# Performance work log

Hardware: AMD Instinct MI355X
Metric: run time of the kernel (lower is better)

The kernel has to match this reference:

```python
import jax, jax.numpy as jnp
import numpy as np

B, S, E, H = 64, 50, 512, 1024
VS, VT, T = 32000, 32000, 50
PAD = 0


def setup_inputs() -> dict:
    key = jax.random.key(0)
    ks = jax.random.split(key, 20)
    p = lambda k, shape: (jax.random.normal(k, shape, dtype=jnp.float32) * 0.02)
    inp = {
        "source_batch": jax.random.randint(ks[0], (B, S), 0, VS),
        "source_lengths": jax.random.randint(ks[1], (B,), 0, S),
        "batch_positions": jax.random.randint(ks[2], (B, S), 0, S + 1),
        "target_batch": jax.random.randint(ks[3], (B, T), 0, VT),
        # encoder params
        "enc_emb": p(ks[4], (VS, E)),
        "pos_emb": p(ks[5], (S + 1, E)),
        "cat_W": p(ks[6], (E, 2 * E)),
        "cat_b": p(ks[7], (E,)),
        "scale_W": p(ks[8], (H, E)),
        "scale_b": p(ks[9], (H,)),
        # decoder params
        "dec_emb": p(ks[10], (VT, E)),
        "attn_W": p(ks[11], (1, H + E)),
        "attn_b": p(ks[12], (1,)),
        "W_ih": p(ks[13], (4 * H, 2 * E)),
        "W_hh": p(ks[14], (4 * H, H)),
        "b_ih": p(ks[15], (4 * H,)),
        "b_hh": p(ks[16], (4 * H,)),
        "proj_W": p(ks[17], (VT, H)),
        "proj_b": p(ks[18], (VT,)),
    }
    return inp


def _forward(source_batch, batch_positions, target_batch,
             enc_emb, pos_emb, cat_W, cat_b, scale_W, scale_b,
             dec_emb, attn_W, attn_b, W_ih, W_hh, b_ih, b_hh, proj_W, proj_b):
    # ---- Encoder (GRU is unused in the original forward; dropout = eval identity)
    words = enc_emb[source_batch]            # (B,S,E)
    pos = pos_emb[batch_positions]           # (B,S,E)
    cat = jnp.concatenate([words, pos], axis=2)            # (B,S,2E)
    enc_out = cat @ cat_W.T + cat_b                         # (B,S,E)
    avg = jnp.mean(enc_out, axis=1)                         # (B,E)
    h0 = jax.nn.relu(avg @ scale_W.T + scale_b)             # (B,H)
    pad_mask = (source_batch == PAD)[..., None]             # (B,S,1)

    Hd = h0.shape[1]

    def step(carry, tok):
        h, c = carry                                        # (B,H), (B,H)
        w = dec_emb[tok]                                    # (B,E)
        rep_h = jnp.broadcast_to(h[:, None, :], (h.shape[0], S, Hd))
        attn_in = jnp.concatenate([enc_out, rep_h], axis=2)  # (B,S,E+H)
        scores = attn_in @ attn_W.T + attn_b                 # (B,S,1)
        aw = jax.nn.softmax(scores, axis=1)                  # softmax over S
        aw = jnp.where(pad_mask, 0.0, aw)
        aw = aw / jnp.sum(aw, axis=1, keepdims=True)
        ctx = jnp.sum(aw * enc_out, axis=1)                  # (B,E)
        x = jnp.concatenate([w, ctx], axis=1)                # (B,2E)
        gates = x @ W_ih.T + b_ih + h @ W_hh.T + b_hh        # (B,4H)
        i, f, g, o = jnp.split(gates, 4, axis=1)
        i, f, o = jax.nn.sigmoid(i), jax.nn.sigmoid(f), jax.nn.sigmoid(o)
        g = jnp.tanh(g)
        c_new = f * c + i * g
        h_new = o * jnp.tanh(c_new)
        logits = h_new @ proj_W.T + proj_b                   # (B,VT)
        return (h_new, c_new), logits

    toks = target_batch[:, : T - 1].T                        # (T-1, B)
    _, logits = jax.lax.scan(step, (h0, h0), toks)
    return logits                                            # (T-1, B, VT)


def reference(source_batch, source_lengths, batch_positions, target_batch,
              enc_emb, pos_emb, cat_W, cat_b, scale_W, scale_b,
              dec_emb, attn_W, attn_b, W_ih, W_hh, b_ih, b_hh, proj_W, proj_b):
    del source_lengths  # only used for max_len, which is unused downstream
    return _forward(source_batch, batch_positions, target_batch,
                    enc_emb, pos_emb, cat_W, cat_b, scale_W, scale_b,
                    dec_emb, attn_W, attn_b, W_ih, W_hh, b_ih, b_hh, proj_W, proj_b)
```

## Files before the change

kernel.cpp:

```cpp
#include <hip/hip_runtime.h>
#include <hip/hip_bf16.h>


typedef __attribute__((ext_vector_type(8))) short bf16x8;
typedef __attribute__((ext_vector_type(4))) short short4v;
typedef __attribute__((ext_vector_type(4))) float f32x4;

__device__ __forceinline__ short f2b(float f) {
    union { float f; unsigned u; } x;
    x.f = f;
    unsigned r = (x.u + 0x7FFFu + ((x.u >> 16) & 1u)) >> 16;
    return (short)r;
}
__device__ __forceinline__ float b2f(short s) {
    union { unsigned u; float f; } x;
    x.u = ((unsigned)(unsigned short)s) << 16;
    return x.f;
}

__global__ __launch_bounds__(256)
void cvt_kernel(const float* __restrict__ in, short* __restrict__ out, int n4) {
    int i = blockIdx.x * 256 + threadIdx.x;
    if (i < n4) {
        float4 x = ((const float4*)in)[i];
        short4v v;
        v[0] = f2b(x.x); v[1] = f2b(x.y); v[2] = f2b(x.z); v[3] = f2b(x.w);
        ((short4v*)out)[i] = v;
    }
}

template <int MODE>
__global__ __launch_bounds__(256, 2)
void gemm_bt(const float* __restrict__ Af, const float* __restrict__ Af2,
             const short* __restrict__ Ab,
             const int* __restrict__ idx1, const int* __restrict__ idx2,
             const short* __restrict__ Bt,
             const float* __restrict__ bias1, const float* __restrict__ bias2,
             float* __restrict__ Out) {
    constexpr int OUTS = (MODE == 0) ? 512 : ((MODE == 1) ? 4096 : 32000);

    __shared__ short As[128 * 32];
    __shared__ short Bs[128 * 32];

    const int tid = threadIdx.x;
    const int lane = tid & 63;
    const int wave = tid >> 6;
    const int wm = wave >> 1, wn = wave & 1;
    const int quad = lane >> 4;
    const int l15 = lane & 15;
    const int tm = blockIdx.y * 128;
    const int tn = blockIdx.x * 128;

    f32x4 acc[4][4];
    const f32x4 vzero = {0.f, 0.f, 0.f, 0.f};
#pragma unroll
    for (int mi = 0; mi < 4; mi++)
#pragma unroll
        for (int ni = 0; ni < 4; ni++) acc[mi][ni] = vzero;

    const int c0 = tid, c1 = tid + 256;
    const int r0 = c0 >> 2, r1 = c1 >> 2;
    const int o0 = (c0 & 3) * 8, o1 = (c1 & 3) * 8;

    const float *a0_lo = nullptr, *a0_hi = nullptr, *a1_lo = nullptr, *a1_hi = nullptr;
    const short *ab0 = nullptr, *ab1 = nullptr;
    if constexpr (MODE == 0) {
        const int g0 = tm + r0, g1 = tm + r1;
        a0_lo = Af + idx1[g0] * 512;
        a0_hi = Af2 + idx2[g0] * 512 - 512;
        a1_lo = Af + idx1[g1] * 512;
        a1_hi = Af2 + idx2[g1] * 512 - 512;
    } else if constexpr (MODE == 1) {
        int g0 = tm + r0; if (g0 > 3135) g0 = 3135;
        int g1 = tm + r1; if (g1 > 3135) g1 = 3135;
        a0_lo = Af + idx1[(g0 & 63) * 50 + (g0 >> 6)] * 512;
        a0_hi = Af2 + (g0 & 63) * 512 - 512;
        a1_lo = Af + idx1[(g1 & 63) * 50 + (g1 >> 6)] * 512;
        a1_hi = Af2 + (g1 & 63) * 512 - 512;
    } else {
        ab0 = Ab + (tm + r0) * 1024;
        ab1 = Ab + (tm + r1) * 1024;
    }
    const short* pb0 = Bt + (tn + r0) * 1024;
    const short* pb1 = Bt + (tn + r1) * 1024;

    for (int k0 = 0; k0 < 1024; k0 += 32) {
        const int ka0 = k0 + o0, ka1 = k0 + o1;
        bf16x8 va0, va1;
        if constexpr (MODE == 2) {
            va0 = *(const bf16x8*)(ab0 + ka0);
            va1 = *(const bf16x8*)(ab1 + ka1);
        } else {
            const float* p0 = (ka0 < 512) ? (a0_lo + ka0) : (a0_hi + ka0);
            const float* p1 = (ka1 < 512) ? (a1_lo + ka1) : (a1_hi + ka1);
            float4 x0 = *(const float4*)p0, y0 = *(const float4*)(p0 + 4);
            float4 x1 = *(const float4*)p1, y1 = *(const float4*)(p1 + 4);
            va0[0] = f2b(x0.x); va0[1] = f2b(x0.y); va0[2] = f2b(x0.z); va0[3] = f2b(x0.w);
            va0[4] = f2b(y0.x); va0[5] = f2b(y0.y); va0[6] = f2b(y0.z); va0[7] = f2b(y0.w);
            va1[0] = f2b(x1.x); va1[1] = f2b(x1.y); va1[2] = f2b(x1.z); va1[3] = f2b(x1.w);
            va1[4] = f2b(y1.x); va1[5] = f2b(y1.y); va1[6] = f2b(y1.z); va1[7] = f2b(y1.w);
        }
        bf16x8 vb0 = *(const bf16x8*)(pb0 + ka0);
        bf16x8 vb1 = *(const bf16x8*)(pb1 + ka1);

        __syncthreads();
        *(bf16x8*)&As[r0 * 32 + o0] = va0;
        *(bf16x8*)&As[r1 * 32 + o1] = va1;
        *(bf16x8*)&Bs[r0 * 32 + o0] = vb0;
        *(bf16x8*)&Bs[r1 * 32 + o1] = vb1;
        __syncthreads();

        bf16x8 af[4], bfr[4];
#pragma unroll
        for (int mi = 0; mi < 4; mi++)
            af[mi] = *(const bf16x8*)&As[(wm * 64 + mi * 16 + l15) * 32 + quad * 8];
#pragma unroll
        for (int ni = 0; ni < 4; ni++)
            bfr[ni] = *(const bf16x8*)&Bs[(wn * 64 + ni * 16 + l15) * 32 + quad * 8];
#pragma unroll
        for (int mi = 0; mi < 4; mi++)
#pragma unroll
            for (int ni = 0; ni < 4; ni++)
                acc[mi][ni] = __builtin_amdgcn_mfma_f32_16x16x32_bf16(
                    af[mi], bfr[ni], acc[mi][ni], 0, 0, 0);
    }

    const int gm_base = tm + wm * 64;
    const int gn_base = tn + wn * 64;
#pragma unroll
    for (int mi = 0; mi < 4; mi++) {
#pragma unroll
        for (int ni = 0; ni < 4; ni++) {
            const int gn = gn_base + ni * 16 + l15;
            float bias = bias1[gn];
            if constexpr (MODE == 1) bias += bias2[gn];
#pragma unroll
            for (int r = 0; r < 4; r++) {
                const int gm = gm_base + mi * 16 + quad * 4 + r;
                float v = acc[mi][ni][r] + bias;
                if constexpr (MODE == 0) {
                    Out[gm * OUTS + gn] = v;
                } else {
                    if (gm < 3136) Out[gm * OUTS + gn] = v;
                }
            }
        }
    }
}

__global__ __launch_bounds__(256)
void h0_kernel(const float* __restrict__ enc, const float* __restrict__ sW,
               const float* __restrict__ sb, short* __restrict__ h0out,
               float* __restrict__ cst) {
    __shared__ float avg[512];
    const int b = blockIdx.x;
    const int tid = threadIdx.x;
    for (int e = tid; e < 512; e += 256) {
        float s = 0.f;
        for (int ss = 0; ss < 50; ss++) s += enc[(b * 50 + ss) * 512 + e];
        avg[e] = s * (1.0f / 50.0f);
    }
    __syncthreads();
    for (int r = tid; r < 1024; r += 256) {
        float s = sb[r];
        const float* wr = sW + r * 512;
        for (int e = 0; e < 512; e++) s += avg[e] * wr[e];
        s = fmaxf(s, 0.f);
        h0out[b * 1024 + r] = f2b(s);
        cst[b * 1024 + r] = s;
    }
}

__global__ __launch_bounds__(256)
void attn_kernel(const float* __restrict__ enc, const float* __restrict__ attn_W,
                 const int* __restrict__ src, float* __restrict__ ctx) {
    __shared__ float wE[512];
    __shared__ float part[64][4];
    __shared__ float aws[64];
    const int b = blockIdx.x;
    const int tid = threadIdx.x;
    for (int e = tid; e < 512; e += 256) wE[e] = attn_W[e];
    __syncthreads();
    const int ss = tid >> 2, q = tid & 3;
    float p = 0.f;
    if (ss < 50) {
        const float* row = enc + (b * 50 + ss) * 512;
        for (int e = q * 128; e < q * 128 + 128; e++) p += row[e] * wE[e];
    }
    part[ss][q] = p;
    __syncthreads();
    if (tid < 64) aws[tid] = part[tid][0] + part[tid][1] + part[tid][2] + part[tid][3];
    __syncthreads();
    if (tid == 0) {
        float mx = -1e30f;
        for (int s = 0; s < 50; s++) mx = fmaxf(mx, aws[s]);
        float sum = 0.f;
        for (int s = 0; s < 50; s++) {
            float v = (src[b * 50 + s] == 0) ? 0.f : expf(aws[s] - mx);
            aws[s] = v;
            sum += v;
        }
        float inv = 1.f / sum;
        for (int s = 0; s < 50; s++) aws[s] *= inv;
    }
    __syncthreads();
    for (int e = tid; e < 512; e += 256) {
        float s = 0.f;
        for (int ss2 = 0; ss2 < 50; ss2++) s += aws[ss2] * enc[(b * 50 + ss2) * 512 + e];
        ctx[b * 512 + e] = s;
    }
}

__global__ __launch_bounds__(256)
void lstm_step(const short* __restrict__ hprev, short* __restrict__ hnext,
               const float* __restrict__ pre_t, const short* __restrict__ whh,
               float* __restrict__ cst) {
    __shared__ float gsm[16 * 64];
    const int tid = threadIdx.x;
    const int lane = tid & 63;
    const int w = tid >> 6;
    const int quad = lane >> 4;
    const int l15 = lane & 15;
    const int j0 = blockIdx.x * 4;

    const short* arow = whh + ((l15 >> 2) * 1024 + j0 + (l15 & 3)) * 1024;
    const short* brow = hprev + (w * 16 + l15) * 1024;
    f32x4 acc = {0.f, 0.f, 0.f, 0.f};
#pragma unroll
    for (int k0 = 0; k0 < 1024; k0 += 32) {
        bf16x8 a = *(const bf16x8*)(arow + k0 + quad * 8);
        bf16x8 bb = *(const bf16x8*)(brow + k0 + quad * 8);
        acc = __builtin_amdgcn_mfma_f32_16x16x32_bf16(a, bb, acc, 0, 0, 0);
    }
#pragma unroll
    for (int r = 0; r < 4; r++) gsm[(quad * 4 + r) * 64 + w * 16 + l15] = acc[r];
    __syncthreads();

    const int b = tid & 63;
    const int jl = tid >> 6;
    const int j = j0 + jl;
    float gi = gsm[(0 + jl) * 64 + b] + pre_t[b * 4096 + j];
    float gf = gsm[(4 + jl) * 64 + b] + pre_t[b * 4096 + 1024 + j];
    float gg = gsm[(8 + jl) * 64 + b] + pre_t[b * 4096 + 2048 + j];
    float go = gsm[(12 + jl) * 64 + b] + pre_t[b * 4096 + 3072 + j];
    float iv = 1.f / (1.f + expf(-gi));
    float fv = 1.f / (1.f + expf(-gf));
    float gv = tanhf(gg);
    float ov = 1.f / (1.f + expf(-go));
    const int ci = b * 1024 + j;
    float cn = fv * cst[ci] + iv * gv;
    cst[ci] = cn;
    hnext[ci] = f2b(ov * tanhf(cn));
}

extern "C" void kernel_launch(void* const* d_in, const int* in_sizes, int n_in,
                              void* d_out, int out_size, void* d_ws, size_t ws_size,
                              hipStream_t stream) {
    (void)in_sizes; (void)n_in; (void)out_size; (void)ws_size;

    const int* src = (const int*)d_in[0];
    const int* pos = (const int*)d_in[2];
    const int* tgt = (const int*)d_in[3];
    const float* enc_emb = (const float*)d_in[4];
    const float* pos_emb = (const float*)d_in[5];
    const float* cat_W = (const float*)d_in[6];
    const float* cat_b = (const float*)d_in[7];
    const float* scale_W = (const float*)d_in[8];
    const float* scale_b = (const float*)d_in[9];
    const float* dec_emb = (const float*)d_in[10];
    const float* attn_W = (const float*)d_in[11];
    const float* W_ih = (const float*)d_in[13];
    const float* W_hh = (const float*)d_in[14];
    const float* b_ih = (const float*)d_in[15];
    const float* b_hh = (const float*)d_in[16];
    const float* proj_W = (const float*)d_in[17];
    const float* proj_b = (const float*)d_in[18];
    float* out = (float*)d_out;

    char* ws = (char*)d_ws;
    short* H_ALL = (short*)(ws + 0);
    float* ENCO  = (float*)(ws + 6684672);
    float* CST   = (float*)(ws + 13238272);
    float* CTX   = (float*)(ws + 13500416);
    float* PRE   = (float*)(ws + 13631488);
    short* CATW  = (short*)(ws + 65011712);
    short* WIH   = (short*)(ws + 66060288);
    short* WHH   = (short*)(ws + 74448896);
    short* PROJ  = (short*)(ws + 82837504);

    cvt_kernel<<<512, 256, 0, stream>>>(cat_W, CATW, 131072);
    cvt_kernel<<<4096, 256, 0, stream>>>(W_ih, WIH, 1048576);
    cvt_kernel<<<4096, 256, 0, stream>>>(W_hh, WHH, 1048576);
    cvt_kernel<<<32000, 256, 0, stream>>>(proj_W, PROJ, 8192000);

    gemm_bt<0><<<dim3(4, 25), 256, 0, stream>>>(enc_emb, pos_emb, nullptr, src, pos,
                                                CATW, cat_b, nullptr, ENCO);
    h0_kernel<<<64, 256, 0, stream>>>(ENCO, scale_W, scale_b, H_ALL, CST);
    attn_kernel<<<64, 256, 0, stream>>>(ENCO, attn_W, src, CTX);
    gemm_bt<1><<<dim3(32, 25), 256, 0, stream>>>(dec_emb, CTX, nullptr, tgt, nullptr,
                                                 WIH, b_ih, b_hh, PRE);
    for (int t = 0; t < 49; t++)
        lstm_step<<<256, 256, 0, stream>>>(H_ALL + t * 65536, H_ALL + (t + 1) * 65536,
                                           PRE + t * 64 * 4096, WHH, CST);
    gemm_bt<2><<<dim3(250, 25), 256, 0, stream>>>(nullptr, nullptr, H_ALL + 65536,
                                                  nullptr, nullptr, PROJ, proj_b, nullptr, out);
}
```

Before: 1.631 ms.

## Use direct global-to-LDS loads, XCD-aware tile swizzle, and vectorize h0 dot product

Loads of the bf16 B tiles, and of the A tiles in mode 2, now go straight from global memory into LDS through global_load_lds. This skips the round trip through registers. Block-to-tile mapping for the gate and projection GEMMs is remapped so consecutive blocks on the same XCD share tiles, aiming at better L2 reuse. The h0 kernel's dot product is vectorized with float4 loads. The direct LDS loads are issued after the barrier, so their latency is no longer overlapped with the previous iteration, and the swizzle arithmetic assumes fixed grid sizes.

```diff
diff --git a/kernel.cpp b/kernel.cpp
--- a/kernel.cpp
+++ b/kernel.cpp
@@ -12,10 +12,12 @@
     unsigned r = (x.u + 0x7FFFu + ((x.u >> 16) & 1u)) >> 16;
     return (short)r;
 }
-__device__ __forceinline__ float b2f(short s) {
-    union { unsigned u; float f; } x;
-    x.u = ((unsigned)(unsigned short)s) << 16;
-    return x.f;
+
+__device__ __forceinline__ void gload16(const short* g, short* l) {
+    __builtin_amdgcn_global_load_lds(
+        (const __attribute__((address_space(1))) unsigned int*)g,
+        (__attribute__((address_space(3))) unsigned int*)l,
+        16, 0, 0);
 }
 
 __global__ __launch_bounds__(256)
@@ -48,8 +50,22 @@
     const int wm = wave >> 1, wn = wave & 1;
     const int quad = lane >> 4;
     const int l15 = lane & 15;
-    const int tm = blockIdx.y * 128;
-    const int tn = blockIdx.x * 128;
+
+    int mt, nt;
+    if constexpr (MODE == 0) {
+        mt = blockIdx.y; nt = blockIdx.x;
+    } else if constexpr (MODE == 1) {
+        const int f = blockIdx.y * 32 + blockIdx.x;
+        const int g = (f & 7) * 100 + (f >> 3);
+        mt = g % 25; nt = g / 25;
+    } else {
+        const int f = blockIdx.y * 250 + blockIdx.x;
+        const int xcd = f & 7, rk = f >> 3;
+        const int g = (xcd < 2) ? xcd * 782 + rk : 1564 + (xcd - 2) * 781 + rk;
+        mt = g % 25; nt = g / 25;
+    }
+    const int tm = mt * 128;
+    const int tn = nt * 128;
 
     f32x4 acc[4][4];
     const f32x4 vzero = {0.f, 0.f, 0.f, 0.f};
@@ -87,10 +103,7 @@
     for (int k0 = 0; k0 < 1024; k0 += 32) {
         const int ka0 = k0 + o0, ka1 = k0 + o1;
         bf16x8 va0, va1;
-        if constexpr (MODE == 2) {
-            va0 = *(const bf16x8*)(ab0 + ka0);
-            va1 = *(const bf16x8*)(ab1 + ka1);
-        } else {
+        if constexpr (MODE != 2) {
             const float* p0 = (ka0 < 512) ? (a0_lo + ka0) : (a0_hi + ka0);
             const float* p1 = (ka1 < 512) ? (a1_lo + ka1) : (a1_hi + ka1);
             float4 x0 = *(const float4*)p0, y0 = *(const float4*)(p0 + 4);
@@ -100,14 +113,17 @@
             va1[0] = f2b(x1.x); va1[1] = f2b(x1.y); va1[2] = f2b(x1.z); va1[3] = f2b(x1.w);
             va1[4] = f2b(y1.x); va1[5] = f2b(y1.y); va1[6] = f2b(y1.z); va1[7] = f2b(y1.w);
         }
-        bf16x8 vb0 = *(const bf16x8*)(pb0 + ka0);
-        bf16x8 vb1 = *(const bf16x8*)(pb1 + ka1);
 
         __syncthreads();
-        *(bf16x8*)&As[r0 * 32 + o0] = va0;
-        *(bf16x8*)&As[r1 * 32 + o1] = va1;
-        *(bf16x8*)&Bs[r0 * 32 + o0] = vb0;
-        *(bf16x8*)&Bs[r1 * 32 + o1] = vb1;
+        gload16(pb0 + ka0, &Bs[r0 * 32 + o0]);
+        gload16(pb1 + ka1, &Bs[r1 * 32 + o1]);
+        if constexpr (MODE == 2) {
+            gload16(ab0 + ka0, &As[r0 * 32 + o0]);
+            gload16(ab1 + ka1, &As[r1 * 32 + o1]);
+        } else {
+            *(bf16x8*)&As[r0 * 32 + o0] = va0;
+            *(bf16x8*)&As[r1 * 32 + o1] = va1;
+        }
         __syncthreads();
 
         bf16x8 af[4], bfr[4];
@@ -163,8 +179,13 @@
     __syncthreads();
     for (int r = tid; r < 1024; r += 256) {
         float s = sb[r];
-        const float* wr = sW + r * 512;
-        for (int e = 0; e < 512; e++) s += avg[e] * wr[e];
+        const float4* wr = (const float4*)(sW + r * 512);
+        const float4* av = (const float4*)avg;
+#pragma unroll 4
+        for (int e = 0; e < 128; e++) {
+            float4 w = wr[e], a = av[e];
+            s += w.x * a.x + w.y * a.y + w.z * a.z + w.w * a.w;
+        }
         s = fmaxf(s, 0.f);
         h0out[b * 1024 + r] = f2b(s);
         cst[b * 1024 + r] = s;
```

Result: no change. 1.625 ms (-0.4%).
